# Optimization experiments

Hardware: AMD Instinct MI355X
Metric: run time of the kernel (lower is better)

The kernel has to match this reference:

```python
import jax, jax.numpy as jnp
import numpy as np

N, A, H, W = 8, 256, 128, 128
C = 19            # number of real classes (fc rows)
CP1 = 20          # estimator classes = class_num + 1
HT, WT = 1024, 1024


def setup_inputs() -> dict:
    key = jax.random.key(0)
    k1, k2, k3, k4 = jax.random.split(key, 4)
    return {
        "features": jax.random.normal(k1, (N, A, H, W), dtype=jnp.float32),
        "y": jax.random.normal(k2, (N, C, H, W), dtype=jnp.float32),
        "fc_weight": jax.random.normal(k3, (C, A), dtype=jnp.float32) * 0.05,
        "Ave": jnp.zeros((CP1, A), jnp.float32),
        "CoVariance": jnp.zeros((CP1, A), jnp.float32),
        "Amount": jnp.zeros((CP1,), jnp.float32),
        "target": jax.random.randint(k4, (N, HT, WT), 0, C, dtype=jnp.int64),
        "ratio": 5,
    }


def reference(features, y, fc_weight, Ave, CoVariance, Amount, target, ratio):
    n, a, h, w = features.shape
    ht, wt = target.shape[1], target.shape[2]
    # nearest-neighbor downsample of labels: src_idx = floor(dst * in/out)
    ih = (jnp.arange(h) * ht) // h
    iw = (jnp.arange(w) * wt) // w
    tgt = target[:, ih][:, :, iw]                       # [N,H,W]

    feats = features.transpose(0, 2, 3, 1).reshape(-1, a)   # [NHW, A]
    y2 = y.transpose(0, 2, 3, 1).reshape(-1, C)              # [NHW, C]
    labels = tgt.reshape(-1)                                  # [NHW]

    mask255 = labels == 255
    lab0 = jnp.where(mask255, 0, labels)                      # 255 -> 0

    # ---- EstimatorCV.update_CV: per-class scatter mean / variance ----
    f = jax.lax.stop_gradient(feats)
    counts = jnp.zeros((CP1,), f.dtype).at[lab0].add(1.0)     # [CP1]
    counts_c = jnp.where(counts == 0, 1.0, counts)
    sums = jnp.zeros((CP1, a), f.dtype).at[lab0].add(f)
    ave = sums / counts_c[:, None]                            # [CP1, A]
    var = jnp.zeros((CP1, a), f.dtype).at[lab0].add((f - ave[lab0]) ** 2)
    var = var / counts_c[:, None]

    denom = counts + Amount
    wcv = jnp.where(denom > 0, counts / denom, 0.0)[:, None]  # [CP1,1]
    new_cov = CoVariance * (1 - wcv) + var * wcv + wcv * (1 - wcv) * (Ave - ave) ** 2
    new_cov = jax.lax.stop_gradient(new_cov)                  # .detach() in torch

    # ---- isda_aug: sigma2[n,c] = ratio * sum_a (W[c]-W[l_n])^2 * CV[l_n] ----
    Wm = fc_weight                                            # [C, A]
    CVl = new_cov[lab0]                                       # [NHW, A]
    Wl = Wm[lab0]                                             # [NHW, A]
    sigma2 = ratio * (
        CVl @ (Wm ** 2).T
        - 2.0 * (CVl * Wl) @ Wm.T
        + jnp.sum(Wl ** 2 * CVl, axis=-1, keepdims=True)
    )                                                          # [NHW, C]

    keep = (1.0 - mask255.astype(y2.dtype))[:, None]
    aug = y2 + 0.5 * sigma2 * keep
    return aug.reshape(n, h, w, C).transpose(0, 3, 1, 2)
```

## Files before the change

kernel.cpp:

```cpp
#include <hip/hip_runtime.h>
#include <stdint.h>

#define NB   8
#define AB   256
#define HB   128
#define WB   128
#define CB   19
#define CP1  20
#define PLANE (HB*WB)
#define NPIX  (NB*PLANE)
#define NREP 8

typedef __attribute__((ext_vector_type(8))) short bf8_t;
typedef __attribute__((ext_vector_type(4))) float f4_t;
union ABu { bf8_t v; unsigned short u[8]; };

__device__ inline unsigned short f2bf(float f) {
    unsigned int u = __float_as_uint(f);
    return (unsigned short)((u + 0x7FFFu + ((u >> 16) & 1u)) >> 16);
}

__global__ __launch_bounds__(256) void k_labels(const int* __restrict__ target,
                                                unsigned char* __restrict__ labels,
                                                unsigned char* __restrict__ lab0,
                                                float* __restrict__ counts) {
    __shared__ int hist[CP1];
    int tid = threadIdx.x;
    if (tid < CP1) hist[tid] = 0;
    __syncthreads();

    int p = blockIdx.x * 256 + tid;
    int n   = p >> 14;
    int rem = p & 16383;
    int h   = rem >> 7;
    int w   = rem & 127;
    size_t idx = (size_t)n * 1048576 + (size_t)h * 8192 + (size_t)w * 8;
    int l = target[idx];
    labels[p] = (unsigned char)l;
    int m = (l == 255) ? 0 : ((l >= 0 && l < CP1) ? l : 0);
    lab0[p] = (unsigned char)m;
    atomicAdd(&hist[m], 1);
    __syncthreads();
    if (tid < CP1) atomicAdd(&counts[tid], (float)hist[tid]);
}

__global__ __launch_bounds__(256) void k_stats(const float* __restrict__ features,
                                               const unsigned char* __restrict__ lab0,
                                               float* __restrict__ gsumR,
                                               float* __restrict__ gsqR) {
    __shared__ uint2 labs[64];
    const int tid  = threadIdx.x;
    const int lane = tid & 63;
    const int w    = tid >> 6;

    const int bx = blockIdx.x;
    const int cg = bx & 3;
    const int pc = (bx >> 2) & 31;
    const int n  = bx >> 7;
    const int rep = bx & (NREP - 1);

    if (tid < 64)
        labs[tid] = ((const uint2*)(lab0 + (size_t)n * PLANE + pc * 512))[tid];
    __syncthreads();

    const int col = lane & 15;
    const int pg  = (lane >> 4) * 8;
    const int ch  = cg * 64 + w * 16 + col;
    const float* fbase = features + ((size_t)(n * AB + ch)) * PLANE + pc * 512 + pg;

    f4_t aS0 = {0.f,0.f,0.f,0.f}, aQ0 = {0.f,0.f,0.f,0.f};
    f4_t aS1 = {0.f,0.f,0.f,0.f}, aQ1 = {0.f,0.f,0.f,0.f};

    const unsigned int t0 = (unsigned int)col;
    const unsigned int t1 = 16u + (unsigned int)col;

    #pragma unroll 4
    for (int t = 0; t < 16; ++t) {
        float4 va = *(const float4*)(fbase + t * 32);
        float4 vb = *(const float4*)(fbase + t * 32 + 4);
        uint2 lw = labs[(t * 32 + pg) >> 3];
        unsigned int bb[8] = { lw.x & 255u, (lw.x >> 8) & 255u, (lw.x >> 16) & 255u, lw.x >> 24,
                               lw.y & 255u, (lw.y >> 8) & 255u, (lw.y >> 16) & 255u, lw.y >> 24 };
        float fv[8] = { va.x, va.y, va.z, va.w, vb.x, vb.y, vb.z, vb.w };
        ABu a0, a1, bs, bq;
        #pragma unroll
        for (int j = 0; j < 8; ++j) {
            a0.u[j] = (bb[j] == t0) ? (unsigned short)0x3F80 : (unsigned short)0;
            a1.u[j] = (bb[j] == t1) ? (unsigned short)0x3F80 : (unsigned short)0;
            bs.u[j] = f2bf(fv[j]);
            bq.u[j] = f2bf(fv[j] * fv[j]);
        }
        aS0 = __builtin_amdgcn_mfma_f32_16x16x32_bf16(a0.v, bs.v, aS0, 0, 0, 0);
        aS1 = __builtin_amdgcn_mfma_f32_16x16x32_bf16(a1.v, bs.v, aS1, 0, 0, 0);
        aQ0 = __builtin_amdgcn_mfma_f32_16x16x32_bf16(a0.v, bq.v, aQ0, 0, 0, 0);
        aQ1 = __builtin_amdgcn_mfma_f32_16x16x32_bf16(a1.v, bq.v, aQ1, 0, 0, 0);
    }

    float* gs = gsumR + rep * (CP1 * 256);
    float* gq = gsqR  + rep * (CP1 * 256);
    const int rbase = (lane >> 4) * 4;
    #pragma unroll
    for (int r = 0; r < 4; ++r) {
        atomicAdd(&gs[(rbase + r) * 256 + ch], aS0[r]);
        atomicAdd(&gq[(rbase + r) * 256 + ch], aQ0[r]);
    }
    if (rbase == 0) {
        #pragma unroll
        for (int r = 0; r < 4; ++r) {
            atomicAdd(&gs[(16 + r) * 256 + ch], aS1[r]);
            atomicAdd(&gq[(16 + r) * 256 + ch], aQ1[r]);
        }
    }
}

__global__ __launch_bounds__(256) void k_table(const float* __restrict__ counts,
                                               const float* __restrict__ gsumR,
                                               const float* __restrict__ gsqR,
                                               const float* __restrict__ fcw,
                                               const float* __restrict__ Ave,
                                               const float* __restrict__ CoV,
                                               const float* __restrict__ Amount,
                                               const int* __restrict__ ratio_p,
                                               float* __restrict__ table) {
    __shared__ float ncov_s[256];
    __shared__ float wl_s[256];
    int t = threadIdx.x;
    int l = blockIdx.x;

    float sum = 0.f, sq = 0.f;
    #pragma unroll
    for (int r = 0; r < NREP; ++r) {
        sum += gsumR[r * (CP1 * 256) + l * 256 + t];
        sq  += gsqR [r * (CP1 * 256) + l * 256 + t];
    }

    float cnt  = counts[l];
    float cntc = (cnt == 0.f) ? 1.f : cnt;
    float ave  = sum / cntc;
    float var  = sq / cntc - ave * ave;
    float denom = cnt + Amount[l];
    float wcv  = (denom > 0.f) ? cnt / denom : 0.f;
    float d0   = Ave[l * 256 + t] - ave;
    float ncov = CoV[l * 256 + t] * (1.f - wcv) + var * wcv + wcv * (1.f - wcv) * d0 * d0;

    ncov_s[t] = ncov;
    int lwr = (l < CB) ? l : (CB - 1);
    wl_s[t] = fcw[lwr * 256 + t];
    __syncthreads();

    int wv = t >> 6, lane = t & 63;
    float ratio_f = (float)(*ratio_p);
    for (int c = wv; c < CB; c += 4) {
        float4 nc = *(const float4*)&ncov_s[lane * 4];
        float4 wl = *(const float4*)&wl_s[lane * 4];
        float4 wc = *(const float4*)&fcw[c * 256 + lane * 4];
        float e0 = wc.x - wl.x, e1 = wc.y - wl.y, e2 = wc.z - wl.z, e3 = wc.w - wl.w;
        float r = nc.x * e0 * e0 + nc.y * e1 * e1 + nc.z * e2 * e2 + nc.w * e3 * e3;
        #pragma unroll
        for (int off = 32; off; off >>= 1) r += __shfl_down(r, off);
        if (lane == 0) table[l * CB + c] = ratio_f * r;
    }
}

__global__ __launch_bounds__(256) void k_apply(const float* __restrict__ y,
                                               const unsigned char* __restrict__ labels,
                                               const float* __restrict__ table,
                                               float* __restrict__ out) {
    __shared__ float tab[CP1 * CB];
    int tid = threadIdx.x;
    for (int i = tid; i < CP1 * CB; i += 256) tab[i] = table[i];
    __syncthreads();

    int b = blockIdx.x;
    int chunk = b & 3;
    int c = (b >> 2) % CB;
    int n = b / (4 * CB);

    const float* ybase = y + ((size_t)(n * CB + c)) * PLANE;
    float* obase = out + ((size_t)(n * CB + c)) * PLANE;
    const unsigned char* lbase = labels + (size_t)n * PLANE;

    #pragma unroll
    for (int it = 0; it < 4; ++it) {
        int pix = chunk * 4096 + it * 1024 + tid * 4;
        float4 yv = *reinterpret_cast<const float4*>(ybase + pix);
        unsigned int lwv = *reinterpret_cast<const unsigned int*>(lbase + pix);
        float ya[4] = {yv.x, yv.y, yv.z, yv.w};
        float o[4];
        #pragma unroll
        for (int j = 0; j < 4; ++j) {
            int l = (lwv >> (8 * j)) & 255;
            bool keep = (l != 255);
            int lab0i = keep ? (l < CP1 ? l : 0) : 0;
            float s = tab[lab0i * CB + c];
            o[j] = ya[j] + (keep ? 0.5f * s : 0.f);
        }
        *reinterpret_cast<float4*>(obase + pix) = make_float4(o[0], o[1], o[2], o[3]);
    }
}

extern "C" void kernel_launch(void* const* d_in, const int* in_sizes, int n_in,
                              void* d_out, int out_size, void* d_ws, size_t ws_size,
                              hipStream_t stream) {
    const float* features = (const float*)d_in[0];
    const float* y        = (const float*)d_in[1];
    const float* fcw      = (const float*)d_in[2];
    const float* Ave      = (const float*)d_in[3];
    const float* CoV      = (const float*)d_in[4];
    const float* Amount   = (const float*)d_in[5];
    const int*   target   = (const int*)d_in[6];
    const int*   ratio    = (const int*)d_in[7];

    char* ws = (char*)d_ws;
    float* counts = (float*)(ws + 0);
    float* gsumR  = (float*)(ws + 128);
    float* gsqR   = (float*)(ws + 128 + 163840);
    unsigned char* labels = (unsigned char*)(ws + 327808);
    unsigned char* lab0   = (unsigned char*)(ws + 458880);
    float* table  = (float*)(ws + 589952);
    float* out    = (float*)d_out;

    hipMemsetAsync(ws, 0, 327808, stream);

    k_labels<<<NPIX / 256,   256, 0, stream>>>(target, labels, lab0, counts);
    k_stats <<<NB * 32 * 4,  256, 0, stream>>>(features, lab0, gsumR, gsqR);
    k_table <<<CP1,          256, 0, stream>>>(counts, gsumR, gsqR, fcw, Ave, CoV, Amount, ratio, table);
    k_apply <<<NB * CB * 4,  256, 0, stream>>>(y, labels, table, out);
}
```

Baseline: 243.1 us.

## Replace global atomic reduction with per-block partials and larger pixel chunks

k_stats now processes 1024 pixels per block instead of 512, which halves the grid. Each block writes its per-class sum and square-sum partials to a private slot in a workspace buffer instead of doing global atomicAdds into 8 replicated buffers. k_table then reduces the 128 partials per channel group. The large memset is cut down to the counts array only. This removes atomic contention and most of the memset, at the cost of a longer serial reduction loop inside the 20-block k_table.

```diff
diff --git a/kernel.cpp b/kernel.cpp
--- a/kernel.cpp
+++ b/kernel.cpp
@@ -9,7 +9,6 @@
 #define CP1  20
 #define PLANE (HB*WB)
 #define NPIX  (NB*PLANE)
-#define NREP 8
 
 typedef __attribute__((ext_vector_type(8))) short bf8_t;
 typedef __attribute__((ext_vector_type(4))) float f4_t;
@@ -46,27 +45,25 @@
 
 __global__ __launch_bounds__(256) void k_stats(const float* __restrict__ features,
                                                const unsigned char* __restrict__ lab0,
-                                               float* __restrict__ gsumR,
-                                               float* __restrict__ gsqR) {
-    __shared__ uint2 labs[64];
+                                               float* __restrict__ gpart) {
+    __shared__ uint2 labs[128];
     const int tid  = threadIdx.x;
     const int lane = tid & 63;
     const int w    = tid >> 6;
 
     const int bx = blockIdx.x;
     const int cg = bx & 3;
-    const int pc = (bx >> 2) & 31;
-    const int n  = bx >> 7;
-    const int rep = bx & (NREP - 1);
-
-    if (tid < 64)
-        labs[tid] = ((const uint2*)(lab0 + (size_t)n * PLANE + pc * 512))[tid];
+    const int pc = (bx >> 2) & 15;
+    const int n  = bx >> 6;
+
+    if (tid < 128)
+        labs[tid] = ((const uint2*)(lab0 + (size_t)n * PLANE + pc * 1024))[tid];
     __syncthreads();
 
     const int col = lane & 15;
     const int pg  = (lane >> 4) * 8;
     const int ch  = cg * 64 + w * 16 + col;
-    const float* fbase = features + ((size_t)(n * AB + ch)) * PLANE + pc * 512 + pg;
+    const float* fbase = features + ((size_t)(n * AB + ch)) * PLANE + pc * 1024 + pg;
 
     f4_t aS0 = {0.f,0.f,0.f,0.f}, aQ0 = {0.f,0.f,0.f,0.f};
     f4_t aS1 = {0.f,0.f,0.f,0.f}, aQ1 = {0.f,0.f,0.f,0.f};
@@ -75,7 +72,7 @@
     const unsigned int t1 = 16u + (unsigned int)col;
 
     #pragma unroll 4
-    for (int t = 0; t < 16; ++t) {
+    for (int t = 0; t < 32; ++t) {
         float4 va = *(const float4*)(fbase + t * 32);
         float4 vb = *(const float4*)(fbase + t * 32 + 4);
         uint2 lw = labs[(t * 32 + pg) >> 3];
@@ -96,26 +93,25 @@
         aQ1 = __builtin_amdgcn_mfma_f32_16x16x32_bf16(a1.v, bq.v, aQ1, 0, 0, 0);
     }
 
-    float* gs = gsumR + rep * (CP1 * 256);
-    float* gq = gsqR  + rep * (CP1 * 256);
+    float* P = gpart + (size_t)bx * (40 * 64);
+    const int chl = w * 16 + col;
     const int rbase = (lane >> 4) * 4;
     #pragma unroll
     for (int r = 0; r < 4; ++r) {
-        atomicAdd(&gs[(rbase + r) * 256 + ch], aS0[r]);
-        atomicAdd(&gq[(rbase + r) * 256 + ch], aQ0[r]);
+        P[(rbase + r) * 64 + chl]      = aS0[r];
+        P[(20 + rbase + r) * 64 + chl] = aQ0[r];
     }
     if (rbase == 0) {
         #pragma unroll
         for (int r = 0; r < 4; ++r) {
-            atomicAdd(&gs[(16 + r) * 256 + ch], aS1[r]);
-            atomicAdd(&gq[(16 + r) * 256 + ch], aQ1[r]);
+            P[(16 + r) * 64 + chl] = aS1[r];
+            P[(36 + r) * 64 + chl] = aQ1[r];
         }
     }
 }
 
 __global__ __launch_bounds__(256) void k_table(const float* __restrict__ counts,
-                                               const float* __restrict__ gsumR,
-                                               const float* __restrict__ gsqR,
+                                               const float* __restrict__ gpart,
                                                const float* __restrict__ fcw,
                                                const float* __restrict__ Ave,
                                                const float* __restrict__ CoV,
@@ -127,11 +123,14 @@
     int t = threadIdx.x;
     int l = blockIdx.x;
 
+    int cg  = t >> 6;
+    int chl = t & 63;
     float sum = 0.f, sq = 0.f;
-    #pragma unroll
-    for (int r = 0; r < NREP; ++r) {
-        sum += gsumR[r * (CP1 * 256) + l * 256 + t];
-        sq  += gsqR [r * (CP1 * 256) + l * 256 + t];
+    #pragma unroll 4
+    for (int npc = 0; npc < 128; ++npc) {
+        const float* P = gpart + (size_t)(cg + 4 * npc) * (40 * 64);
+        sum += P[l * 64 + chl];
+        sq  += P[(20 + l) * 64 + chl];
     }
 
     float cnt  = counts[l];
@@ -213,17 +212,16 @@
 
     char* ws = (char*)d_ws;
     float* counts = (float*)(ws + 0);
-    float* gsumR  = (float*)(ws + 128);
-    float* gsqR   = (float*)(ws + 128 + 163840);
-    unsigned char* labels = (unsigned char*)(ws + 327808);
-    unsigned char* lab0   = (unsigned char*)(ws + 458880);
-    float* table  = (float*)(ws + 589952);
+    float* gpart  = (float*)(ws + 128);
+    unsigned char* labels = (unsigned char*)(ws + 5243008);
+    unsigned char* lab0   = (unsigned char*)(ws + 5374080);
+    float* table  = (float*)(ws + 5505152);
     float* out    = (float*)d_out;
 
-    hipMemsetAsync(ws, 0, 327808, stream);
-
-    k_labels<<<NPIX / 256,   256, 0, stream>>>(target, labels, lab0, counts);
-    k_stats <<<NB * 32 * 4,  256, 0, stream>>>(features, lab0, gsumR, gsqR);
-    k_table <<<CP1,          256, 0, stream>>>(counts, gsumR, gsqR, fcw, Ave, CoV, Amount, ratio, table);
-    k_apply <<<NB * CB * 4,  256, 0, stream>>>(y, labels, table, out);
-}
+    hipMemsetAsync(counts, 0, 128, stream);
+
+    k_labels<<<NPIX / 256,  256, 0, stream>>>(target, labels, lab0, counts);
+    k_stats <<<NB * 16 * 4, 256, 0, stream>>>(features, lab0, gpart);
+    k_table <<<CP1,         256, 0, stream>>>(counts, gpart, fcw, Ave, CoV, Amount, ratio, table);
+    k_apply <<<NB * CB * 4, 256, 0, stream>>>(y, labels, table, out);
+}
```

After: 268.1 us. +10.3%, slower.
